# Optimization experiments

Measured on AMD Instinct MI355X. Metric: run time of the kernel, lower is better.

Reference implementation:

```python
import jax, jax.numpy as jnp
import numpy as np

K_NEIGHBORS = 3  # self.K in DSVDD


def setup_inputs() -> dict:
    key = jax.random.key(0)
    k1, k2 = jax.random.split(key)
    B, N, C = 16, 3136, 112   # batch, h*w patches, descriptor channels
    M = 3136                  # memory-bank size
    phi_p = jax.random.normal(k1, (B, N, C), dtype=jnp.float32)
    C_bank = jax.random.normal(k2, (C, M), dtype=jnp.float32)
    return {"phi_p": phi_p, "C_bank": C_bank, "h": 56}


def reference(phi_p, C_bank, h):
    # squared distances via ||phi||^2 + ||c||^2 - 2 phi.c  -> (B, N, M)
    features = jnp.sum(phi_p * phi_p, axis=2, keepdims=True)        # (B, N, 1)
    centers = jnp.sum(C_bank * C_bank, axis=0, keepdims=True)       # (1, M)
    f_c = 2.0 * jnp.einsum('bnc,cm->bnm', phi_p, C_bank)            # (B, N, M)
    dist = jnp.sqrt(features + centers - f_c)                        # (B, N, M)
    # K smallest distances (ascending, like torch.topk(largest=False))
    neg_topk, _ = jax.lax.top_k(-dist, K_NEIGHBORS)                  # (B, N, K)
    dist_k = -neg_topk
    # softmin over K, take weight of the nearest neighbor times its distance
    softmin0 = jax.nn.softmax(-dist_k, axis=-1)[:, :, 0]             # (B, N)
    score = softmin0 * dist_k[:, :, 0]                               # (B, N)
    B, N = score.shape
    w = N // h
    return score.reshape(B, 1, h, w)  # b c h w with c=1
```

## Files before the change

### kernel.cpp

```cpp
#include <hip/hip_runtime.h>
#include <stdint.h>


typedef short s16x8 __attribute__((ext_vector_type(8)));
typedef float fx4 __attribute__((ext_vector_type(4)));

#define M_TOT 3136
#define CC 112
#define NROWS 50176
#define N_TILES_TOT 50

__device__ __forceinline__ unsigned short f2bf(float x) {
  unsigned u = __float_as_uint(x);
  u += 0x7fffu + ((u >> 16) & 1u);
  return (unsigned short)(u >> 16);
}

#define INSERT3(T0, T1, T2, V)                                  \
  do {                                                          \
    const float _a0 = (T0), _a1 = (T1), _v = (V);               \
    (T0) = fmaxf(_a0, _v);                                      \
    (T1) = __builtin_amdgcn_fmed3f(_a0, _a1, _v);               \
    (T2) = __builtin_amdgcn_fmed3f(_a1, (T2), _v);              \
  } while (0)

__global__ __launch_bounds__(256) void dsvdd_prep(const float* __restrict__ Cb,
                                                  unsigned char* __restrict__ CT2) {
  const int tile = blockIdx.x;
  __shared__ float partial[256];
  __shared__ float c2s[64];
  const int tm = threadIdx.x & 63;
  const int seg = threadIdx.x >> 6;
  const int m = tile * 64 + tm;
  float ss = 0.f;
  if (m < M_TOT) {
    for (int k = seg * 28; k < seg * 28 + 28; ++k) {
      const float x = Cb[(size_t)k * M_TOT + m];
      ss += x * x;
    }
  }
  partial[threadIdx.x] = ss;
  __syncthreads();
  if (seg == 0) {
    const float c2 = partial[tm] + partial[64 + tm] + partial[128 + tm] + partial[192 + tm];
    c2s[tm] = (m < M_TOT) ? (-0.125f * c2) : -2500.0f;
  }
  __syncthreads();
#pragma unroll
  for (int it = 0; it < 4; ++it) {
    const int s = it * 256 + threadIdx.x;
    const int f = s >> 8;
    const int ks = (s >> 6) & 3;
    const int l = s & 63;
    const int mloc = f * 16 + (l & 15);
    const int mm = tile * 64 + mloc;
    const bool mv = (mm < M_TOT);
    const int k0 = ks * 32 + (l >> 4) * 8;
    float v[8];
#pragma unroll
    for (int j = 0; j < 8; ++j) {
      const int k = k0 + j;
      float x = 0.f;
      if (k < CC) x = mv ? Cb[(size_t)k * M_TOT + mm] : 0.f;
      else if (k < 116) x = c2s[mloc];
      v[j] = x;
    }
    uint4 pk;
    pk.x = (unsigned)f2bf(v[0]) | ((unsigned)f2bf(v[1]) << 16);
    pk.y = (unsigned)f2bf(v[2]) | ((unsigned)f2bf(v[3]) << 16);
    pk.z = (unsigned)f2bf(v[4]) | ((unsigned)f2bf(v[5]) << 16);
    pk.w = (unsigned)f2bf(v[6]) | ((unsigned)f2bf(v[7]) << 16);
    *(uint4*)(CT2 + (size_t)tile * 16384 + (size_t)s * 16) = pk;
  }
}

__global__ __launch_bounds__(256, 3) void dsvdd_stage1(const float* __restrict__ phi,
                                                       const unsigned char* __restrict__ CT2,
                                                       float* __restrict__ part,
                                                       float* __restrict__ featg, int nT) {
  __shared__ __align__(16) unsigned char phiF[32768];
  float(*const mg)[8] = (float(*)[8])phiF;

  const int t = threadIdx.x;
  const int lane = t & 63;
  const int w = t >> 6;
  const int g = w >> 1;
  const int h = w & 1;
  const int cq = lane & 15;
  const int kq = lane >> 4;
  const int c = blockIdx.y;
  const int tile0 = c * nT;
  const long rowBase = (long)blockIdx.x * 128;
  const bool needF = (c == 0);

  {
    const int r = t >> 1;
    const int h2 = t & 1;
    const float* src = phi + (size_t)(rowBase + r) * CC + h2 * 56;
    unsigned char* const base = phiF + (((r >> 4) * 4) * 1024);
    const int pcq = r & 15;
    float ss = 0.f;
#pragma unroll
    for (int j = 0; j < 7; ++j) {
      const int k0 = h2 * 56 + j * 8;
      const int ks = k0 >> 5;
      const int kqw = (k0 >> 3) & 3;
      const float4 a = *(const float4*)(src + j * 8);
      const float4 b = *(const float4*)(src + j * 8 + 4);
      ss += a.x * a.x + a.y * a.y + a.z * a.z + a.w * a.w;
      ss += b.x * b.x + b.y * b.y + b.z * b.z + b.w * b.w;
      uint4 pk;
      pk.x = (unsigned)f2bf(a.x) | ((unsigned)f2bf(a.y) << 16);
      pk.y = (unsigned)f2bf(a.z) | ((unsigned)f2bf(a.w) << 16);
      pk.z = (unsigned)f2bf(b.x) | ((unsigned)f2bf(b.y) << 16);
      pk.w = (unsigned)f2bf(b.z) | ((unsigned)f2bf(b.w) << 16);
      *(uint4*)(base + ks * 1024 + (kqw * 16 + pcq) * 16) = pk;
    }
    {
      uint4 pk;
      if (h2 == 0) { pk.x = 0x3f803f80u; pk.y = 0x3f803f80u; pk.z = 0u; pk.w = 0u; }
      else { pk.x = pk.y = pk.z = pk.w = 0u; }
      *(uint4*)(base + 3 * 1024 + ((2 + h2) * 16 + pcq) * 16) = pk;
    }
    ss += __shfl_xor(ss, 1);
    if (needF && h2 == 0) featg[rowBase + r] = ss;
  }
  __syncthreads();

  s16x8 bg[4][4];
#pragma unroll
  for (int ks = 0; ks < 4; ++ks)
#pragma unroll
    for (int pf = 0; pf < 4; ++pf)
      bg[ks][pf] = *(const s16x8*)(phiF + (((g * 4 + pf) * 4 + ks) * 64 + lane) * 16);
  __syncthreads();

  float t0[4], t1[4], t2[4];
#pragma unroll
  for (int pf = 0; pf < 4; ++pf) t0[pf] = t1[pf] = t2[pf] = -3.0e38f;

  const unsigned char* ap = CT2 + (size_t)(h * 2) * 4096 + (size_t)lane * 16;
  s16x8 afA[8], afB[8];

#define LOADAF(DST, TIDX)                                                     \
  do {                                                                        \
    const unsigned char* _p = ap + (size_t)(TIDX)*16384;                      \
    _Pragma("unroll") for (int mf = 0; mf < 2; ++mf)                          \
        _Pragma("unroll") for (int ks = 0; ks < 4; ++ks)                      \
            DST[mf * 4 + ks] = *(const s16x8*)(_p + mf * 4096 + ks * 1024);   \
  } while (0)

#define COMPUTE(SRC)                                                          \
  do {                                                                        \
    const fx4 _zz = {0.f, 0.f, 0.f, 0.f};                                     \
    _Pragma("unroll") for (int mf = 0; mf < 2; ++mf) {                        \
      fx4 acc[4];                                                             \
      _Pragma("unroll") for (int ks = 0; ks < 4; ++ks)                        \
          _Pragma("unroll") for (int pf = 0; pf < 4; ++pf)                    \
              acc[pf] = __builtin_amdgcn_mfma_f32_16x16x32_bf16(              \
                  SRC[mf * 4 + ks], bg[ks][pf], (ks == 0) ? _zz : acc[pf],    \
                  0, 0, 0);                                                   \
      _Pragma("unroll") for (int pf = 0; pf < 4; ++pf)                        \
          _Pragma("unroll") for (int rg = 0; rg < 4; ++rg)                    \
              INSERT3(t0[pf], t1[pf], t2[pf], acc[pf][rg]);                   \
    }                                                                         \
  } while (0)

  LOADAF(afA, tile0);
  int tt = 0;
  while (tt + 2 < nT) {
    LOADAF(afB, tile0 + tt + 1);
    COMPUTE(afA);
    LOADAF(afA, tile0 + tt + 2);
    COMPUTE(afB);
    tt += 2;
  }
  if (tt + 1 < nT) {
    LOADAF(afB, tile0 + tt + 1);
    COMPUTE(afA);
    COMPUTE(afB);
  } else {
    COMPUTE(afA);
  }
#undef LOADAF
#undef COMPUTE

#pragma unroll
  for (int pf = 0; pf < 4; ++pf) {
#pragma unroll
    for (int off = 16; off < 64; off <<= 1) {
      const float b0 = __shfl_xor(t0[pf], off);
      const float b1 = __shfl_xor(t1[pf], off);
      const float b2 = __shfl_xor(t2[pf], off);
      INSERT3(t0[pf], t1[pf], t2[pf], b0);
      INSERT3(t0[pf], t1[pf], t2[pf], b1);
      INSERT3(t0[pf], t1[pf], t2[pf], b2);
    }
  }
  if (kq == 0) {
#pragma unroll
    for (int pf = 0; pf < 4; ++pf) {
      const int row = g * 64 + pf * 16 + cq;
      mg[row][h * 3 + 0] = t0[pf];
      mg[row][h * 3 + 1] = t1[pf];
      mg[row][h * 3 + 2] = t2[pf];
    }
  }
  __syncthreads();
  if (t < 128) {
    float s0 = mg[t][0], s1 = mg[t][1], s2 = mg[t][2];
    INSERT3(s0, s1, s2, mg[t][3]);
    INSERT3(s0, s1, s2, mg[t][4]);
    INSERT3(s0, s1, s2, mg[t][5]);
    float* dst = part + ((size_t)c * NROWS + rowBase + t) * 3;
    dst[0] = s0; dst[1] = s1; dst[2] = s2;
  }
}

__global__ __launch_bounds__(256) void dsvdd_stage2(const float* __restrict__ part,
                                                    const float* __restrict__ featg,
                                                    float* __restrict__ out, int S) {
  const int row = blockIdx.x * 256 + threadIdx.x;
  if (row >= NROWS) return;
  float s0 = -3.0e38f, s1 = -3.0e38f, s2 = -3.0e38f;
  for (int c = 0; c < S; ++c) {
    const float* p = part + ((size_t)c * NROWS + row) * 3;
    INSERT3(s0, s1, s2, p[0]);
    INSERT3(s0, s1, s2, p[1]);
    INSERT3(s0, s1, s2, p[2]);
  }
  const float feat = featg[row];
  const float d0 = sqrtf(fmaxf(feat - 2.f * s0, 0.f));
  const float d1 = sqrtf(fmaxf(feat - 2.f * s1, 0.f));
  const float d2 = sqrtf(fmaxf(feat - 2.f * s2, 0.f));
  const float w0 = 1.0f / (1.0f + __expf(d0 - d1) + __expf(d0 - d2));
  out[row] = w0 * d0;
}

extern "C" void kernel_launch(void* const* d_in, const int* in_sizes, int n_in,
                              void* d_out, int out_size, void* d_ws, size_t ws_size,
                              hipStream_t stream) {
  (void)in_sizes; (void)n_in; (void)out_size;
  const float* phi = (const float*)d_in[0];
  const float* Cb = (const float*)d_in[1];
  float* out = (float*)d_out;
  unsigned char* CT2 = (unsigned char*)d_ws;
  float* featg = (float*)((unsigned char*)d_ws + 819200);
  float* partp = (float*)((unsigned char*)d_ws + 819200 + 200704);
  const size_t base = 819200 + 200704;
  int S = 1;
  if (ws_size >= base + (size_t)5 * NROWS * 12) S = 5;
  else if (ws_size >= base + (size_t)2 * NROWS * 12) S = 2;
  const int nT = N_TILES_TOT / S;
  dsvdd_prep<<<50, 256, 0, stream>>>(Cb, CT2);
  dsvdd_stage1<<<dim3(392, S), 256, 0, stream>>>(phi, CT2, partp, featg, nT);
  dsvdd_stage2<<<196, 256, 0, stream>>>(partp, featg, out, S);
}
```

Baseline: 63.45 us.

## Stage bank tiles through LDS with async global-to-LDS double buffering

Replaces the per-wave register double-buffered global loads of the memory-bank tiles with global_load_lds async copies into two shared 16KB LDS buffers. Each wave loads a quarter of the tile and two waves share it, with explicit vmcnt waits and barriers around each compute step. Tile order is rotated per block to spread L2 traffic, and occupancy is raised from 3 to 4 blocks per SM. The aim is to halve redundant global loads, free registers and overlap copies with MFMA work. The cost is two block barriers per tile and extra LDS read traffic.

New measurement: 64.69 us. About the same (+2.0%).

```diff
diff --git a/kernel.cpp b/kernel.cpp
--- a/kernel.cpp
+++ b/kernel.cpp
@@ -14,6 +14,12 @@
   unsigned u = __float_as_uint(x);
   u += 0x7fffu + ((u >> 16) & 1u);
   return (unsigned short)(u >> 16);
+}
+
+__device__ __forceinline__ void async16(const void* g, void* l) {
+  __builtin_amdgcn_global_load_lds(
+      (const __attribute__((address_space(1))) unsigned int*)g,
+      (__attribute__((address_space(3))) unsigned int*)l, 16, 0, 0);
 }
 
 #define INSERT3(T0, T1, T2, V)                                  \
@@ -74,12 +80,12 @@
   }
 }
 
-__global__ __launch_bounds__(256, 3) void dsvdd_stage1(const float* __restrict__ phi,
+__global__ __launch_bounds__(256, 4) void dsvdd_stage1(const float* __restrict__ phi,
                                                        const unsigned char* __restrict__ CT2,
                                                        float* __restrict__ part,
                                                        float* __restrict__ featg, int nT) {
-  __shared__ __align__(16) unsigned char phiF[32768];
-  float(*const mg)[8] = (float(*)[8])phiF;
+  __shared__ __align__(16) unsigned char lds[32768];
+  float(*const mg)[8] = (float(*)[8])lds;
 
   const int t = threadIdx.x;
   const int lane = t & 63;
@@ -90,14 +96,15 @@
   const int kq = lane >> 4;
   const int c = blockIdx.y;
   const int tile0 = c * nT;
-  const long rowBase = (long)blockIdx.x * 128;
+  const int bid = (int)blockIdx.x;
+  const long rowBase = (long)bid * 128;
   const bool needF = (c == 0);
 
   {
     const int r = t >> 1;
     const int h2 = t & 1;
     const float* src = phi + (size_t)(rowBase + r) * CC + h2 * 56;
-    unsigned char* const base = phiF + (((r >> 4) * 4) * 1024);
+    unsigned char* const base = lds + ((r >> 4) * 4096);
     const int pcq = r & 15;
     float ss = 0.f;
 #pragma unroll
@@ -132,58 +139,67 @@
   for (int ks = 0; ks < 4; ++ks)
 #pragma unroll
     for (int pf = 0; pf < 4; ++pf)
-      bg[ks][pf] = *(const s16x8*)(phiF + (((g * 4 + pf) * 4 + ks) * 64 + lane) * 16);
-  __syncthreads();
+      bg[ks][pf] = *(const s16x8*)(lds + ((g * 4 + pf) * 4 + ks) * 1024 + lane * 16);
+  __syncthreads();
+
+#define STAGE(BUF, TIDX)                                                        \
+  do {                                                                          \
+    const unsigned char* _g =                                                   \
+        CT2 + (size_t)(TIDX)*16384 + w * 4096 + (size_t)lane * 16;              \
+    unsigned char* _l = lds + (BUF)*16384 + w * 4096;                           \
+    _Pragma("unroll") for (int i = 0; i < 4; ++i)                               \
+        async16(_g + i * 1024, _l + i * 1024);                                  \
+  } while (0)
+
+#define COMPUTE(BUF)                                                            \
+  do {                                                                          \
+    const unsigned char* _rd = lds + (BUF)*16384 + h * 8192 + lane * 16;        \
+    const fx4 _zz = {0.f, 0.f, 0.f, 0.f};                                       \
+    _Pragma("unroll") for (int mf = 0; mf < 2; ++mf) {                          \
+      s16x8 af[4];                                                              \
+      _Pragma("unroll") for (int ks = 0; ks < 4; ++ks)                          \
+          af[ks] = *(const s16x8*)(_rd + mf * 4096 + ks * 1024);                \
+      fx4 acc[4];                                                               \
+      _Pragma("unroll") for (int ks = 0; ks < 4; ++ks)                          \
+          _Pragma("unroll") for (int pf = 0; pf < 4; ++pf)                      \
+              acc[pf] = __builtin_amdgcn_mfma_f32_16x16x32_bf16(                \
+                  af[ks], bg[ks][pf], (ks == 0) ? _zz : acc[pf], 0, 0, 0);      \
+      _Pragma("unroll") for (int pf = 0; pf < 4; ++pf)                          \
+          _Pragma("unroll") for (int rg = 0; rg < 4; ++rg)                      \
+              INSERT3(t0[pf], t1[pf], t2[pf], acc[pf][rg]);                     \
+    }                                                                           \
+  } while (0)
+
+#define FENCE() __builtin_amdgcn_sched_barrier(0)
 
   float t0[4], t1[4], t2[4];
 #pragma unroll
   for (int pf = 0; pf < 4; ++pf) t0[pf] = t1[pf] = t2[pf] = -3.0e38f;
 
-  const unsigned char* ap = CT2 + (size_t)(h * 2) * 4096 + (size_t)lane * 16;
-  s16x8 afA[8], afB[8];
-
-#define LOADAF(DST, TIDX)                                                     \
-  do {                                                                        \
-    const unsigned char* _p = ap + (size_t)(TIDX)*16384;                      \
-    _Pragma("unroll") for (int mf = 0; mf < 2; ++mf)                          \
-        _Pragma("unroll") for (int ks = 0; ks < 4; ++ks)                      \
-            DST[mf * 4 + ks] = *(const s16x8*)(_p + mf * 4096 + ks * 1024);   \
-  } while (0)
-
-#define COMPUTE(SRC)                                                          \
-  do {                                                                        \
-    const fx4 _zz = {0.f, 0.f, 0.f, 0.f};                                     \
-    _Pragma("unroll") for (int mf = 0; mf < 2; ++mf) {                        \
-      fx4 acc[4];                                                             \
-      _Pragma("unroll") for (int ks = 0; ks < 4; ++ks)                        \
-          _Pragma("unroll") for (int pf = 0; pf < 4; ++pf)                    \
-              acc[pf] = __builtin_amdgcn_mfma_f32_16x16x32_bf16(              \
-                  SRC[mf * 4 + ks], bg[ks][pf], (ks == 0) ? _zz : acc[pf],    \
-                  0, 0, 0);                                                   \
-      _Pragma("unroll") for (int pf = 0; pf < 4; ++pf)                        \
-          _Pragma("unroll") for (int rg = 0; rg < 4; ++rg)                    \
-              INSERT3(t0[pf], t1[pf], t2[pf], acc[pf][rg]);                   \
-    }                                                                         \
-  } while (0)
-
-  LOADAF(afA, tile0);
-  int tt = 0;
-  while (tt + 2 < nT) {
-    LOADAF(afB, tile0 + tt + 1);
-    COMPUTE(afA);
-    LOADAF(afA, tile0 + tt + 2);
-    COMPUTE(afB);
-    tt += 2;
-  }
-  if (tt + 1 < nT) {
-    LOADAF(afB, tile0 + tt + 1);
-    COMPUTE(afA);
-    COMPUTE(afB);
-  } else {
-    COMPUTE(afA);
-  }
-#undef LOADAF
+  {
+    const int j0 = bid % nT;
+    const int j1 = (bid + 1) % nT;
+    STAGE(0, tile0 + j0);
+    STAGE(1, tile0 + j1);
+  }
+  for (int tt = 0; tt < nT; ++tt) {
+    if (tt + 1 < nT) {
+      asm volatile("s_waitcnt vmcnt(4)" ::: "memory");
+    } else {
+      asm volatile("s_waitcnt vmcnt(0)" ::: "memory");
+    }
+    FENCE();
+    __builtin_amdgcn_s_barrier();
+    FENCE();
+    COMPUTE(tt & 1);
+    FENCE();
+    __builtin_amdgcn_s_barrier();
+    FENCE();
+    if (tt + 2 < nT) STAGE(tt & 1, tile0 + (bid + tt + 2) % nT);
+  }
+#undef STAGE
 #undef COMPUTE
+#undef FENCE
 
 #pragma unroll
   for (int pf = 0; pf < 4; ++pf) {
@@ -197,6 +213,7 @@
       INSERT3(t0[pf], t1[pf], t2[pf], b2);
     }
   }
+  __syncthreads();
   if (kq == 0) {
 #pragma unroll
     for (int pf = 0; pf < 4; ++pf) {
```
